# Optimization experiments

Measured on AMD Instinct MI355X. Metric: run time of the kernel, lower is better.

Reference implementation:

```python
import jax, jax.numpy as jnp
import numpy as np

D_MODEL = 1024
NUM_HEADS = 16
HEAD_DIM = D_MODEL // NUM_HEADS
B, S = 4, 2048
NEG = -1e10


def setup_inputs() -> dict:
    key = jax.random.key(0)
    ks = jax.random.split(key, 10)
    s = 1.0 / np.sqrt(D_MODEL)
    x = jax.random.normal(ks[0], (B, S, D_MODEL), dtype=jnp.float32)
    mask = jnp.ones((B, S, S), dtype=jnp.int32)
    Wq = jax.random.uniform(ks[1], (D_MODEL, D_MODEL), jnp.float32, -s, s)
    bq = jnp.zeros((D_MODEL,), jnp.float32)
    Wk = jax.random.uniform(ks[2], (D_MODEL, D_MODEL), jnp.float32, -s, s)
    bk = jnp.zeros((D_MODEL,), jnp.float32)
    Wv = jax.random.uniform(ks[3], (D_MODEL, D_MODEL), jnp.float32, -s, s)
    bv = jnp.zeros((D_MODEL,), jnp.float32)
    Wo = jax.random.uniform(ks[4], (D_MODEL, D_MODEL), jnp.float32, -s, s)
    bo = jnp.zeros((D_MODEL,), jnp.float32)
    return {"x": x, "mask": mask, "Wq": Wq, "bq": bq, "Wk": Wk, "bk": bk,
            "Wv": Wv, "bv": bv, "Wo": Wo, "bo": bo}


def reference(x, mask, Wq, bq, Wk, bk, Wv, bv, Wo, bo):
    # x: [B,S,D]; projections then split into heads -> [B,H,S,hd]
    def split_heads(t):
        return t.reshape(B, S, NUM_HEADS, HEAD_DIM).transpose(0, 2, 1, 3)

    q = split_heads(x @ Wq + bq)
    k = split_heads(x @ Wk + bk)
    v = split_heads(x @ Wv + bv)
    scale = jnp.sqrt(jnp.float32(HEAD_DIM))
    # energy: [B,H,S,S]
    energy = jnp.einsum('bhqd,bhkd->bhqk', q, k) / scale
    energy = jnp.where(mask[:, None, :, :] == 0, jnp.float32(NEG), energy)
    attn = jax.nn.softmax(energy, axis=-1)
    # dropout is identity in eval mode
    out = jnp.einsum('bhqk,bhkd->bhqd', attn, v)
    out = out.transpose(0, 2, 1, 3).reshape(B, S, D_MODEL)
    return out @ Wo + bo
```

## Files before the change

### kernel.cpp

```cpp
#include <hip/hip_runtime.h>
#include <stdint.h>


#define SS 2048
#define NH 16

typedef __bf16 bf16x8 __attribute__((ext_vector_type(8)));
typedef float f32x4 __attribute__((ext_vector_type(4)));

__device__ __forceinline__ unsigned short f2bf(float f) {
  union { float f; unsigned int u; } v; v.f = f;
  unsigned int u = v.u;
  return (unsigned short)((u + 0x7fffu + ((u >> 16) & 1u)) >> 16);
}

__device__ __forceinline__ unsigned int cvtpk(float a, float b) {
  unsigned int r;
  asm("v_cvt_pk_bf16_f32 %0, %1, %2" : "=v"(r) : "v"(a), "v"(b));
  return r;
}

__device__ __forceinline__ float ex2(float x) {
  float r; asm("v_exp_f32 %0, %1" : "=v"(r) : "v"(x)); return r;
}

__device__ __forceinline__ void swap32(unsigned int& a, unsigned int& b) {
  asm volatile("v_permlane32_swap_b32 %0, %1" : "+v"(a), "+v"(b));
}
__device__ __forceinline__ void swap16(unsigned int& a, unsigned int& b) {
  asm volatile("v_permlane16_swap_b32 %0, %1" : "+v"(a), "+v"(b));
}

__device__ __forceinline__ void gload_lds16(const void* g, void* l) {
  __builtin_amdgcn_global_load_lds(
      (__attribute__((address_space(1))) void*)(void*)g,
      (__attribute__((address_space(3))) void*)l,
      16, 0, 0);
}

__global__ __launch_bounds__(256) void k_conv_x(const float* __restrict__ x,
                                                unsigned short* __restrict__ xb) {
  long i = ((long)blockIdx.x * 256 + threadIdx.x) * 4;
  float4 v = *(const float4*)(x + i);
  uint2 o;
  o.x = cvtpk(v.x, v.y);
  o.y = cvtpk(v.z, v.w);
  *(uint2*)(xb + i) = o;
}

__global__ __launch_bounds__(256) void k_transW(const float* __restrict__ W0,
                                                const float* __restrict__ W1,
                                                const float* __restrict__ W2,
                                                const float* __restrict__ W3,
                                                unsigned short* __restrict__ Wt) {
  const float* W = blockIdx.z == 0 ? W0 : blockIdx.z == 1 ? W1 : blockIdx.z == 2 ? W2 : W3;
  unsigned short* dst = Wt + (size_t)blockIdx.z * 1024 * 1024;
  __shared__ float t[64][65];
  int r0 = blockIdx.y * 64, c0 = blockIdx.x * 64;
  int tr = threadIdx.x >> 6, tc = threadIdx.x & 63;
#pragma unroll
  for (int i = 0; i < 16; i++) {
    int r = tr + i * 4;
    t[r][tc] = W[(size_t)(r0 + r) * 1024 + c0 + tc];
  }
  __syncthreads();
#pragma unroll
  for (int i = 0; i < 16; i++) {
    int r = tr + i * 4;
    dst[(size_t)(c0 + r) * 1024 + r0 + tc] = f2bf(t[tc][r]);
  }
}

__global__ __launch_bounds__(256) void k_maskflags(const int* __restrict__ mask,
                                                   int* __restrict__ flg) {
  int kt = blockIdx.x, qb = blockIdx.y, b = blockIdx.z;
  const int* M = mask + ((size_t)b * SS + qb * 128) * SS + kt * 64;
  int tid = threadIdx.x;
  int ok = 1;
#pragma unroll
  for (int i = 0; i < 8; i++) {
    int r = (tid >> 4) + i * 16;
    int4 v = *(const int4*)(M + (size_t)r * SS + (tid & 15) * 4);
    ok &= (v.x != 0) & (v.y != 0) & (v.z != 0) & (v.w != 0);
  }
  ok = __all(ok) ? 1 : 0;
  __shared__ int s[4];
  if ((tid & 63) == 0) s[tid >> 6] = ok;
  __syncthreads();
  if (tid == 0) flg[((size_t)b * 16 + qb) * 32 + kt] = s[0] & s[1] & s[2] & s[3];
}

template <int EPI>
__global__ __launch_bounds__(256) void k_gemm(const unsigned short* __restrict__ A,
                                              const unsigned short* __restrict__ Bt,
                                              const float* __restrict__ bias,
                                              void* __restrict__ Cout, float scale) {
  constexpr int K = 1024, N = 1024;
  __shared__ unsigned short lA[128 * 64];
  __shared__ unsigned short lB[128 * 64];
  const int tid = threadIdx.x;
  const int lane = tid & 63, wave = tid >> 6;
  const int wr = wave >> 1, wc = wave & 1;
  const int g = lane >> 4, c = lane & 15;

  const int bid = blockIdx.x;
  const int xcd = bid & 7, idx = bid >> 3;
  const int by = xcd * 8 + (idx >> 3), bx = idx & 7;
  const long brow = (long)by * 128, bcol = (long)bx * 128;

  f32x4 acc[4][4] = {};

  int sr[4], sch[4];
#pragma unroll
  for (int j = 0; j < 4; j++) {
    int p = j * 4096 + tid * 16;
    int r = p >> 7;
    int sl = (p >> 4) & 7;
    sr[j] = r;
    sch[j] = (sl ^ (r & 7)) * 8;
  }
  char* lbaseA = (char*)lA + wave * 1024;
  char* lbaseB = (char*)lB + wave * 1024;

  for (int k0 = 0; k0 < K; k0 += 64) {
#pragma unroll
    for (int j = 0; j < 4; j++) {
      gload_lds16(A + (brow + sr[j]) * K + k0 + sch[j], lbaseA + j * 4096);
      gload_lds16(Bt + (bcol + sr[j]) * K + k0 + sch[j], lbaseB + j * 4096);
    }
    __syncthreads();
#pragma unroll
    for (int ks = 0; ks < 2; ks++) {
      bf16x8 af[4], bfr[4];
#pragma unroll
      for (int m = 0; m < 4; m++) {
        int ra = wr * 64 + m * 16 + c;
        af[m] = *(const bf16x8*)((const char*)lA + ra * 128 + ((ks * 64 + g * 16) ^ ((ra & 7) << 4)));
        int rb = wc * 64 + m * 16 + c;
        bfr[m] = *(const bf16x8*)((const char*)lB + rb * 128 + ((ks * 64 + g * 16) ^ ((rb & 7) << 4)));
      }
      __builtin_amdgcn_s_setprio(1);
#pragma unroll
      for (int m = 0; m < 4; m++)
#pragma unroll
        for (int n = 0; n < 4; n++)
          acc[m][n] = __builtin_amdgcn_mfma_f32_16x16x32_bf16(af[m], bfr[n], acc[m][n], 0, 0, 0);
      __builtin_amdgcn_s_setprio(0);
    }
    __syncthreads();
  }

#pragma unroll
  for (int m = 0; m < 4; m++) {
#pragma unroll
    for (int n = 0; n < 4; n++) {
      long row0 = brow + wr * 64 + m * 16 + g * 4;
      long col = bcol + wc * 64 + n * 16 + c;
      float bv = bias[col];
      if (EPI == 0) {
        unsigned short* C = (unsigned short*)Cout;
#pragma unroll
        for (int r = 0; r < 4; r++)
          C[(row0 + r) * N + col] = f2bf((acc[m][n][r] + bv) * scale);
      } else if (EPI == 1) {
        unsigned short* C = (unsigned short*)Cout;
        long b_ = row0 >> 11, s = row0 & 2047;
        size_t base = ((size_t)(b_ * NH + (col >> 6)) * 64 + (col & 63)) * SS + s;
        ushort4 pk;
        pk.x = f2bf(acc[m][n][0] + bv);
        pk.y = f2bf(acc[m][n][1] + bv);
        pk.z = f2bf(acc[m][n][2] + bv);
        pk.w = f2bf(acc[m][n][3] + bv);
        *(ushort4*)(C + base) = pk;
      } else {
        float* C = (float*)Cout;
#pragma unroll
        for (int r = 0; r < 4; r++)
          C[(row0 + r) * N + col] = acc[m][n][r] + bv;
      }
    }
  }
}

__global__ __launch_bounds__(256, 4) void k_flash(const unsigned short* __restrict__ Q,
                                                  const unsigned short* __restrict__ Kb,
                                                  const unsigned short* __restrict__ Vt,
                                                  const int* __restrict__ mask,
                                                  const int* __restrict__ flg,
                                                  unsigned short* __restrict__ O) {
  __shared__ unsigned short lK[3][4096];
  __shared__ unsigned short lV[2][4096];
  const int tid = threadIdx.x, lane = tid & 63, w = tid >> 6;
  const int g = lane >> 4, c = lane & 15;

  const int bid = blockIdx.x;
  const int xcd = bid & 7, jj = bid >> 3;
  const int qb = jj & 15, Ghi = jj >> 4;
  const int G = xcd * 8 + Ghi;
  const int h = G & 15, b = G >> 4;

  const int q0 = qb * 128 + w * 32;
  const long mrow0 = (long)b * SS + q0;

  const unsigned short* Kbase = Kb + (size_t)b * SS * 1024 + h * 64;
  const unsigned short* Vbase = Vt + (size_t)((b * NH + h) * 64) * SS;
  const int* Mbase = mask + ((size_t)b * SS + q0) * SS;
  const int* Fbase = flg + ((size_t)b * 16 + qb) * 32;

  int allok = 1;
#pragma unroll
  for (int i = 0; i < 32; i++) allok &= Fbase[i];
  allok = __builtin_amdgcn_readfirstlane(allok);

  bf16x8 qf[2][2];
#pragma unroll
  for (int rt = 0; rt < 2; rt++)
#pragma unroll
    for (int ks = 0; ks < 2; ks++)
      qf[rt][ks] = *(const bf16x8*)(Q + (mrow0 + rt * 16 + c) * 1024 + h * 64 + ks * 32 + g * 8);

  const int pB = tid * 16;
  const int r0 = pB >> 7;
  const int co = (((pB >> 4) & 7) ^ (r0 & 7)) * 8;
  const unsigned short* gK = Kbase + (size_t)r0 * 1024 + co;
  const unsigned short* gV = Vbase + (size_t)r0 * SS + co;
  const int wb = w * 1024;

  char* sk0 = (char*)&lK[0][0];
  char* sk1 = (char*)&lK[1][0];
  char* sk2 = (char*)&lK[2][0];
  char* sv0 = (char*)&lV[0][0];
  char* sv1 = (char*)&lV[1][0];

#define STAGE_K(kt_, dst_) do { \
    const unsigned short* aK_ = gK + (size_t)(kt_) * (64 * 1024); \
    gload_lds16(aK_, (dst_) + wb); \
    gload_lds16(aK_ + 32 * 1024, (dst_) + wb + 4096); } while (0)
#define STAGE_V(kt_, dst_) do { \
    const unsigned short* aV_ = gV + (size_t)(kt_) * 64; \
    gload_lds16(aV_, (dst_) + wb); \
    gload_lds16(aV_ + 32 * (size_t)SS, (dst_) + wb + 4096); } while (0)

  STAGE_K(0, sk0);
  STAGE_V(0, sv0);
  STAGE_K(1, sk1);

  float mst[2] = {8.0f, 8.0f}, lst[2] = {0.0f, 0.0f};
  f32x4 o[2][4] = {};

  for (int kt = 0; kt < SS / 64; kt++) {
    if (kt < SS / 64 - 1) asm volatile("s_waitcnt vmcnt(2)" ::: "memory");
    else                  asm volatile("s_waitcnt vmcnt(0)" ::: "memory");
    __builtin_amdgcn_s_barrier();
    __builtin_amdgcn_sched_barrier(0);
    if (kt + 1 < SS / 64) STAGE_V(kt + 1, sv1);
    if (kt + 2 < SS / 64) STAGE_K(kt + 2, sk2);

    bf16x8 kf[4][2];
#pragma unroll
    for (int ct = 0; ct < 4; ct++)
#pragma unroll
      for (int ks = 0; ks < 2; ks++)
        kf[ct][ks] = *(const bf16x8*)(sk0 + (ct * 16 + c) * 128 +
                                      ((ks * 64 + g * 16) ^ ((c & 7) << 4)));

    f32x4 sc[2][4];
#pragma unroll
    for (int rt = 0; rt < 2; rt++)
#pragma unroll
      for (int ct = 0; ct < 4; ct++)
#pragma unroll
        for (int r = 0; r < 4; r++) sc[rt][ct][r] = -mst[rt];
    __builtin_amdgcn_s_setprio(1);
#pragma unroll
    for (int ks = 0; ks < 2; ks++)
#pragma unroll
      for (int rt = 0; rt < 2; rt++)
#pragma unroll
        for (int ct = 0; ct < 4; ct++)
          sc[rt][ct] = __builtin_amdgcn_mfma_f32_16x16x32_bf16(kf[ct][ks], qf[rt][ks], sc[rt][ct], 0, 0, 0);
    __builtin_amdgcn_s_setprio(0);

    if (!allok) {
      const int key0 = kt * 64;
#pragma unroll
      for (int rt = 0; rt < 2; rt++)
#pragma unroll
        for (int ct = 0; ct < 4; ct++)
#pragma unroll
          for (int r = 0; r < 4; r++) {
            int mv = Mbase[(size_t)(rt * 16 + c) * SS + key0 + ct * 16 + g * 4 + r];
            if (mv == 0) sc[rt][ct][r] = -1e10f;
          }
    }

    float pm[2];
#pragma unroll
    for (int rt = 0; rt < 2; rt++) {
      f32x4 m4;
#pragma unroll
      for (int r = 0; r < 4; r++)
        m4[r] = fmaxf(fmaxf(sc[rt][0][r], sc[rt][1][r]), fmaxf(sc[rt][2][r], sc[rt][3][r]));
      pm[rt] = fmaxf(fmaxf(m4[0], m4[1]), fmaxf(m4[2], m4[3]));
    }
    if (__any((pm[0] > 8.0f) | (pm[1] > 8.0f))) {
#pragma unroll
      for (int rt = 0; rt < 2; rt++) {
        float tmv = pm[rt];
        tmv = fmaxf(tmv, __shfl_xor(tmv, 16, 64));
        tmv = fmaxf(tmv, __shfl_xor(tmv, 32, 64));
        float dpos = fmaxf(tmv, 0.0f);
        float sf = ex2(-dpos);
        mst[rt] += dpos;
        lst[rt] *= sf;
#pragma unroll
        for (int ct = 0; ct < 4; ct++)
#pragma unroll
          for (int r = 0; r < 4; r++) { o[rt][ct][r] *= sf; sc[rt][ct][r] -= dpos; }
      }
    }

    union PU { unsigned int wd[4]; bf16x8 v; };
    PU pf[2][2];
#pragma unroll
    for (int rt = 0; rt < 2; rt++) {
      f32x4 ts4 = {0.0f, 0.0f, 0.0f, 0.0f};
      unsigned int Wd[4][2];
#pragma unroll
      for (int ct = 0; ct < 4; ct++) {
        f32x4 p;
#pragma unroll
        for (int r = 0; r < 4; r++) {
          p[r] = ex2(sc[rt][ct][r]);
          ts4[r] += p[r];
        }
        Wd[ct][0] = cvtpk(p[0], p[1]);
        Wd[ct][1] = cvtpk(p[2], p[3]);
      }
#pragma unroll
      for (int ks = 0; ks < 2; ks++)
#pragma unroll
        for (int hh = 0; hh < 2; hh++) {
          unsigned int a = Wd[2 * ks][hh], bb = Wd[2 * ks + 1][hh];
          swap32(a, bb);
          swap16(a, bb);
          pf[rt][ks].wd[hh] = a;
          pf[rt][ks].wd[2 + hh] = bb;
        }
      lst[rt] += (ts4[0] + ts4[1]) + (ts4[2] + ts4[3]);
    }

    bf16x8 vf[4][2];
#pragma unroll
    for (int ct = 0; ct < 4; ct++)
#pragma unroll
      for (int ks = 0; ks < 2; ks++)
        vf[ct][ks] = *(const bf16x8*)(sv0 + (ct * 16 + c) * 128 +
                                      ((ks * 64 + g * 16) ^ ((c & 7) << 4)));
    __builtin_amdgcn_s_setprio(1);
#pragma unroll
    for (int rt = 0; rt < 2; rt++)
#pragma unroll
      for (int ct = 0; ct < 4; ct++)
#pragma unroll
        for (int ks = 0; ks < 2; ks++)
          o[rt][ct] = __builtin_amdgcn_mfma_f32_16x16x32_bf16(vf[ct][ks], pf[rt][ks].v, o[rt][ct], 0, 0, 0);
    __builtin_amdgcn_s_setprio(0);

    char* tk = sk0; sk0 = sk1; sk1 = sk2; sk2 = tk;
    char* tv = sv0; sv0 = sv1; sv1 = tv;
  }

#pragma unroll
  for (int rt = 0; rt < 2; rt++) {
    float t = lst[rt];
    t += __shfl_xor(t, 16, 64);
    t += __shfl_xor(t, 32, 64);
    float inv = 1.0f / t;
#pragma unroll
    for (int ct = 0; ct < 4; ct++) {
      uint2 pk;
      pk.x = cvtpk(o[rt][ct][0] * inv, o[rt][ct][1] * inv);
      pk.y = cvtpk(o[rt][ct][2] * inv, o[rt][ct][3] * inv);
      *(uint2*)(O + (mrow0 + rt * 16 + c) * 1024 + h * 64 + ct * 16 + g * 4) = pk;
    }
  }
#undef STAGE_K
#undef STAGE_V
}

extern "C" void kernel_launch(void* const* d_in, const int* in_sizes, int n_in,
                              void* d_out, int out_size, void* d_ws, size_t ws_size,
                              hipStream_t stream) {
  const float* x  = (const float*)d_in[0];
  const int* mask = (const int*)d_in[1];
  const float* Wq = (const float*)d_in[2];
  const float* bq = (const float*)d_in[3];
  const float* Wk = (const float*)d_in[4];
  const float* bk = (const float*)d_in[5];
  const float* Wv = (const float*)d_in[6];
  const float* bv = (const float*)d_in[7];
  const float* Wo = (const float*)d_in[8];
  const float* bo = (const float*)d_in[9];

  char* ws = (char*)d_ws;
  unsigned short* xb = (unsigned short*)ws;
  unsigned short* Wt = (unsigned short*)(ws + (16ull << 20));
  unsigned short* Qb = (unsigned short*)(ws + (24ull << 20));
  unsigned short* Kb = (unsigned short*)(ws + (40ull << 20));
  unsigned short* Vt = (unsigned short*)(ws + (56ull << 20));
  int* flg = (int*)d_out;

  k_conv_x<<<8192, 256, 0, stream>>>(x, xb);
  k_transW<<<dim3(16, 16, 4), 256, 0, stream>>>(Wq, Wk, Wv, Wo, Wt);
  k_maskflags<<<dim3(32, 16, 4), 256, 0, stream>>>(mask, flg);
  k_gemm<0><<<512, 256, 0, stream>>>(xb, Wt, bq, Qb, 0.125f * 1.44269504088896f);
  k_gemm<0><<<512, 256, 0, stream>>>(xb, Wt + (1u << 20), bk, Kb, 1.0f);
  k_gemm<1><<<512, 256, 0, stream>>>(xb, Wt + (2u << 20), bv, Vt, 1.0f);
  k_flash<<<1024, 256, 0, stream>>>(Qb, Kb, Vt, mask, flg, xb);
  k_gemm<2><<<512, 256, 0, stream>>>(xb, Wt + (3u << 20), bo, d_out, 1.0f);
}
```

Measured before the change: 210.9 us.

## Fuse QKV projections into one launch and compute softmax row sums via MFMA

The three Q/K/V projection GEMMs are merged into a single 1536-block launch that picks weights, bias, scale and epilogue from the block index. This removes two launch gaps and lets tail blocks of one projection overlap with the next. In the flash kernel, the per-lane softmax denominator accumulation and the final cross-lane shuffles are replaced by an extra MFMA against a vector of bf16 ones. That moves the sum onto the matrix units, at the cost of one extra MFMA per k-slice and of summing bf16-rounded probabilities.

Result: no change. 210.5 us (-0.2%).

```diff
diff --git a/kernel.cpp b/kernel.cpp
--- a/kernel.cpp
+++ b/kernel.cpp
@@ -90,11 +90,14 @@
   if (tid == 0) flg[((size_t)b * 16 + qb) * 32 + kt] = s[0] & s[1] & s[2] & s[3];
 }
 
-template <int EPI>
-__global__ __launch_bounds__(256) void k_gemm(const unsigned short* __restrict__ A,
-                                              const unsigned short* __restrict__ Bt,
-                                              const float* __restrict__ bias,
-                                              void* __restrict__ Cout, float scale) {
+__global__ __launch_bounds__(256) void k_gemmQKV(const unsigned short* __restrict__ A,
+                                                 const unsigned short* __restrict__ Wt,
+                                                 const float* __restrict__ bq,
+                                                 const float* __restrict__ bk,
+                                                 const float* __restrict__ bv,
+                                                 unsigned short* __restrict__ Qb,
+                                                 unsigned short* __restrict__ Kb,
+                                                 unsigned short* __restrict__ Vtp) {
   constexpr int K = 1024, N = 1024;
   __shared__ unsigned short lA[128 * 64];
   __shared__ unsigned short lB[128 * 64];
@@ -103,10 +106,14 @@
   const int wr = wave >> 1, wc = wave & 1;
   const int g = lane >> 4, c = lane & 15;
 
-  const int bid = blockIdx.x;
-  const int xcd = bid & 7, idx = bid >> 3;
+  const int mat = blockIdx.x >> 9;
+  const int inner = blockIdx.x & 511;
+  const int xcd = inner & 7, idx = inner >> 3;
   const int by = xcd * 8 + (idx >> 3), bx = idx & 7;
   const long brow = (long)by * 128, bcol = (long)bx * 128;
+
+  const unsigned short* Bt = Wt + ((size_t)mat << 20);
+  const float* bias = mat == 0 ? bq : (mat == 1 ? bk : bv);
 
   f32x4 acc[4][4] = {};
 
@@ -150,6 +157,92 @@
     __syncthreads();
   }
 
+  const float scale = (mat == 0) ? 0.180336880111120f  : 1.0f;
+#pragma unroll
+  for (int m = 0; m < 4; m++) {
+#pragma unroll
+    for (int n = 0; n < 4; n++) {
+      long row0 = brow + wr * 64 + m * 16 + g * 4;
+      long col = bcol + wc * 64 + n * 16 + c;
+      float bv_ = bias[col];
+      if (mat == 2) {
+        long b_ = row0 >> 11, s = row0 & 2047;
+        size_t base = ((size_t)(b_ * NH + (col >> 6)) * 64 + (col & 63)) * SS + s;
+        ushort4 pk;
+        pk.x = f2bf(acc[m][n][0] + bv_);
+        pk.y = f2bf(acc[m][n][1] + bv_);
+        pk.z = f2bf(acc[m][n][2] + bv_);
+        pk.w = f2bf(acc[m][n][3] + bv_);
+        *(ushort4*)(Vtp + base) = pk;
+      } else {
+        unsigned short* C = mat ? Kb : Qb;
+#pragma unroll
+        for (int r = 0; r < 4; r++)
+          C[(row0 + r) * N + col] = f2bf((acc[m][n][r] + bv_) * scale);
+      }
+    }
+  }
+}
+
+__global__ __launch_bounds__(256) void k_gemmO(const unsigned short* __restrict__ A,
+                                               const unsigned short* __restrict__ Bt,
+                                               const float* __restrict__ bias,
+                                               float* __restrict__ Cout) {
+  constexpr int K = 1024, N = 1024;
+  __shared__ unsigned short lA[128 * 64];
+  __shared__ unsigned short lB[128 * 64];
+  const int tid = threadIdx.x;
+  const int lane = tid & 63, wave = tid >> 6;
+  const int wr = wave >> 1, wc = wave & 1;
+  const int g = lane >> 4, c = lane & 15;
+
+  const int bid = blockIdx.x;
+  const int xcd = bid & 7, idx = bid >> 3;
+  const int by = xcd * 8 + (idx >> 3), bx = idx & 7;
+  const long brow = (long)by * 128, bcol = (long)bx * 128;
+
+  f32x4 acc[4][4] = {};
+
+  int sr[4], sch[4];
+#pragma unroll
+  for (int j = 0; j < 4; j++) {
+    int p = j * 4096 + tid * 16;
+    int r = p >> 7;
+    int sl = (p >> 4) & 7;
+    sr[j] = r;
+    sch[j] = (sl ^ (r & 7)) * 8;
+  }
+  char* lbaseA = (char*)lA + wave * 1024;
+  char* lbaseB = (char*)lB + wave * 1024;
+
+  for (int k0 = 0; k0 < K; k0 += 64) {
+#pragma unroll
+    for (int j = 0; j < 4; j++) {
+      gload_lds16(A + (brow + sr[j]) * K + k0 + sch[j], lbaseA + j * 4096);
+      gload_lds16(Bt + (bcol + sr[j]) * K + k0 + sch[j], lbaseB + j * 4096);
+    }
+    __syncthreads();
+#pragma unroll
+    for (int ks = 0; ks < 2; ks++) {
+      bf16x8 af[4], bfr[4];
+#pragma unroll
+      for (int m = 0; m < 4; m++) {
+        int ra = wr * 64 + m * 16 + c;
+        af[m] = *(const bf16x8*)((const char*)lA + ra * 128 + ((ks * 64 + g * 16) ^ ((ra & 7) << 4)));
+        int rb = wc * 64 + m * 16 + c;
+        bfr[m] = *(const bf16x8*)((const char*)lB + rb * 128 + ((ks * 64 + g * 16) ^ ((rb & 7) << 4)));
+      }
+      __builtin_amdgcn_s_setprio(1);
+#pragma unroll
+      for (int m = 0; m < 4; m++)
+#pragma unroll
+        for (int n = 0; n < 4; n++)
+          acc[m][n] = __builtin_amdgcn_mfma_f32_16x16x32_bf16(af[m], bfr[n], acc[m][n], 0, 0, 0);
+      __builtin_amdgcn_s_setprio(0);
+    }
+    __syncthreads();
+  }
+
 #pragma unroll
   for (int m = 0; m < 4; m++) {
 #pragma unroll
@@ -157,27 +250,9 @@
       long row0 = brow + wr * 64 + m * 16 + g * 4;
       long col = bcol + wc * 64 + n * 16 + c;
       float bv = bias[col];
-      if (EPI == 0) {
-        unsigned short* C = (unsigned short*)Cout;
-#pragma unroll
-        for (int r = 0; r < 4; r++)
-          C[(row0 + r) * N + col] = f2bf((acc[m][n][r] + bv) * scale);
-      } else if (EPI == 1) {
-        unsigned short* C = (unsigned short*)Cout;
-        long b_ = row0 >> 11, s = row0 & 2047;
-        size_t base = ((size_t)(b_ * NH + (col >> 6)) * 64 + (col & 63)) * SS + s;
-        ushort4 pk;
-        pk.x = f2bf(acc[m][n][0] + bv);
-        pk.y = f2bf(acc[m][n][1] + bv);
-        pk.z = f2bf(acc[m][n][2] + bv);
-        pk.w = f2bf(acc[m][n][3] + bv);
-        *(ushort4*)(C + base) = pk;
-      } else {
-        float* C = (float*)Cout;
-#pragma unroll
-        for (int r = 0; r < 4; r++)
-          C[(row0 + r) * N + col] = acc[m][n][r] + bv;
-      }
+#pragma unroll
+      for (int r = 0; r < 4; r++)
+        Cout[(row0 + r) * N + col] = acc[m][n][r] + bv;
     }
   }
 }
@@ -219,6 +294,10 @@
     for (int ks = 0; ks < 2; ks++)
       qf[rt][ks] = *(const bf16x8*)(Q + (mrow0 + rt * 16 + c) * 1024 + h * 64 + ks * 32 + g * 8);
 
+  union OU { unsigned int u[4]; bf16x8 v; } ones;
+#pragma unroll
+  for (int i = 0; i < 4; i++) ones.u[i] = 0x3F803F80u;
+
   const int pB = tid * 16;
   const int r0 = pB >> 7;
   const int co = (((pB >> 4) & 7) ^ (r0 & 7)) * 8;
@@ -245,7 +324,8 @@
   STAGE_V(0, sv0);
   STAGE_K(1, sk1);
 
-  float mst[2] = {8.0f, 8.0f}, lst[2] = {0.0f, 0.0f};
+  float mst[2] = {8.0f, 8.0f};
+  f32x4 lsum[2] = {};
   f32x4 o[2][4] = {};
 
   for (int kt = 0; kt < SS / 64; kt++) {
@@ -312,7 +392,8 @@
         float dpos = fmaxf(tmv, 0.0f);
         float sf = ex2(-dpos);
         mst[rt] += dpos;
-        lst[rt] *= sf;
+#pragma unroll
+        for (int r = 0; r < 4; r++) lsum[rt][r] *= sf;
 #pragma unroll
         for (int ct = 0; ct < 4; ct++)
 #pragma unroll
@@ -324,16 +405,12 @@
     PU pf[2][2];
 #pragma unroll
     for (int rt = 0; rt < 2; rt++) {
-      f32x4 ts4 = {0.0f, 0.0f, 0.0f, 0.0f};
       unsigned int Wd[4][2];
 #pragma unroll
       for (int ct = 0; ct < 4; ct++) {
         f32x4 p;
 #pragma unroll
-        for (int r = 0; r < 4; r++) {
-          p[r] = ex2(sc[rt][ct][r]);
-          ts4[r] += p[r];
-        }
+        for (int r = 0; r < 4; r++) p[r] = ex2(sc[rt][ct][r]);
         Wd[ct][0] = cvtpk(p[0], p[1]);
         Wd[ct][1] = cvtpk(p[2], p[3]);
       }
@@ -347,7 +424,6 @@
           pf[rt][ks].wd[hh] = a;
           pf[rt][ks].wd[2 + hh] = bb;
         }
-      lst[rt] += (ts4[0] + ts4[1]) + (ts4[2] + ts4[3]);
     }
 
     bf16x8 vf[4][2];
@@ -361,10 +437,12 @@
 #pragma unroll
     for (int rt = 0; rt < 2; rt++)
 #pragma unroll
-      for (int ct = 0; ct < 4; ct++)
-#pragma unroll
-        for (int ks = 0; ks < 2; ks++)
+      for (int ks = 0; ks < 2; ks++) {
+        lsum[rt] = __builtin_amdgcn_mfma_f32_16x16x32_bf16(ones.v, pf[rt][ks].v, lsum[rt], 0, 0, 0);
+#pragma unroll
+        for (int ct = 0; ct < 4; ct++)
           o[rt][ct] = __builtin_amdgcn_mfma_f32_16x16x32_bf16(vf[ct][ks], pf[rt][ks].v, o[rt][ct], 0, 0, 0);
+      }
     __builtin_amdgcn_s_setprio(0);
 
     char* tk = sk0; sk0 = sk1; sk1 = sk2; sk2 = tk;
@@ -373,10 +451,7 @@
 
 #pragma unroll
   for (int rt = 0; rt < 2; rt++) {
-    float t = lst[rt];
-    t += __shfl_xor(t, 16, 64);
-    t += __shfl_xor(t, 32, 64);
-    float inv = 1.0f / t;
+    float inv = 1.0f / lsum[rt][0];
 #pragma unroll
     for (int ct = 0; ct < 4; ct++) {
       uint2 pk;
@@ -414,9 +489,7 @@
   k_conv_x<<<8192, 256, 0, stream>>>(x, xb);
   k_transW<<<dim3(16, 16, 4), 256, 0, stream>>>(Wq, Wk, Wv, Wo, Wt);
   k_maskflags<<<dim3(32, 16, 4), 256, 0, stream>>>(mask, flg);
-  k_gemm<0><<<512, 256, 0, stream>>>(xb, Wt, bq, Qb, 0.125f * 1.44269504088896f);
-  k_gemm<0><<<512, 256, 0, stream>>>(xb, Wt + (1u << 20), bk, Kb, 1.0f);
-  k_gemm<1><<<512, 256, 0, stream>>>(xb, Wt + (2u << 20), bv, Vt, 1.0f);
+  k_gemmQKV<<<1536, 256, 0, stream>>>(xb, Wt, bq, bk, bv, Qb, Kb, Vt);
   k_flash<<<1024, 256, 0, stream>>>(Qb, Kb, Vt, mask, flg, xb);
-  k_gemm<2><<<512, 256, 0, stream>>>(xb, Wt + (3u << 20), bo, d_out, 1.0f);
-}
+  k_gemmO<<<512, 256, 0, stream>>>(xb, Wt + (3u << 20), bo, (float*)d_out);
+}
```
